# Kernel tuning notes

Hardware: AMD Instinct MI355X
Metric: run time of the kernel (lower is better)

Reference implementation:

```python
import jax, jax.numpy as jnp
import numpy as np

N = 40000      # num nodes (num_a + num_b)
DA = 128       # emb_size_a
DB = 128       # emb_size_b
E = 640000     # edges per sign (avg degree 16)
K = 3          # spectral_transform_layer
JA, JB = 1.0, 1.0  # Jacobi_paper (a, b)
EPS = 1e-5     # BatchNorm1d eps


def spmm(index, value, n, x):
    # torch_sparse.spmm: out[row] += value * x[col]
    row, col = index[0], index[1]
    return jax.ops.segment_sum(x[col] * value[:, None], row, num_segments=n)


def jacobi_last(x0, idx, val, k, a, b):
    # Jacobi polynomial basis recurrence; returns xs[k-1]
    n = x0.shape[0]
    xs = [x0]
    if k >= 2:
        x1 = ((a - b) / 2) * x0 + ((a + b + 2) / 2) * spmm(idx, val, n, x0)
        xs.append(x1)
    for L in range(2, k):
        c1 = (2 * L + a + b - 1) * (2 * L + a + b) / (2 * L) / (L + a + b)
        c2 = (2 * L + a + b - 1) * (a * a - b * b) / (2 * L) / (L + a + b) / (2 * L + a + b - 2)
        c3 = (L + a) * (L + b) * (2 * L + a + b) / L / (L + a + b) / (2 * L + a + b - 2)
        xn = c1 * spmm(idx, val, n, xs[-1]) + c2 * xs[-1] - c3 * xs[-2]
        xs.append(xn)
    return xs[-1]


def batchnorm(x, g, beta):
    # training-mode BatchNorm1d: batch stats, biased variance
    mu = jnp.mean(x, axis=0)
    var = jnp.var(x, axis=0)
    return g * (x - mu) * jax.lax.rsqrt(var + EPS) + beta


def prelu(x, w):
    return jnp.where(x >= 0, x, w * x)


def setup_inputs() -> dict:
    key = jax.random.key(0)
    ks = jax.random.split(key, 10)
    s = 1.0 / np.sqrt(DA)
    return {
        "x": jax.random.normal(ks[0], (N, DA), dtype=jnp.float32),
        "pos_index": jax.random.randint(ks[1], (2, E), 0, N, dtype=jnp.int64 if jax.config.jax_enable_x64 else jnp.int32),
        "pos_weight": jax.random.uniform(ks[2], (E,), dtype=jnp.float32),
        "neg_index": jax.random.randint(ks[3], (2, E), 0, N, dtype=jnp.int64 if jax.config.jax_enable_x64 else jnp.int32),
        "neg_weight": jax.random.uniform(ks[4], (E,), dtype=jnp.float32),
        "W_org": jax.random.uniform(ks[5], (DA, DB), jnp.float32, -s, s),
        "W_pos": jax.random.uniform(ks[6], (DA, DB), jnp.float32, -s, s),
        "W_neg": jax.random.uniform(ks[7], (DA, DB), jnp.float32, -s, s),
        "g_org": jnp.ones((DB,), jnp.float32), "b_org": jnp.zeros((DB,), jnp.float32),
        "g_pos": jnp.ones((DB,), jnp.float32), "b_pos": jnp.zeros((DB,), jnp.float32),
        "g_neg": jnp.ones((DB,), jnp.float32), "b_neg": jnp.zeros((DB,), jnp.float32),
        "prelu_w": jnp.full((1,), 0.25, jnp.float32),
        "W_mlp": jax.random.uniform(ks[8], (3 * DB, DB), jnp.float32, -1.0 / np.sqrt(3 * DB), 1.0 / np.sqrt(3 * DB)),
    }


def reference(x, pos_index, pos_weight, neg_index, neg_weight,
              W_org, W_pos, W_neg, g_org, b_org, g_pos, b_pos, g_neg, b_neg,
              prelu_w, W_mlp):
    x_org = x @ W_org                      # [N, DB]
    x_pos = x @ W_pos
    x_neg = x @ W_neg
    # dropout p=0 -> identity
    x_pos = jacobi_last(x_pos, pos_index, pos_weight, K, JA, JB)
    x_neg = jacobi_last(x_neg, neg_index, neg_weight, K, JA, JB)
    x_org = batchnorm(x_org, g_org, b_org)  # alpha3 = 1
    x_pos = batchnorm(x_pos, g_pos, b_pos)
    x_neg = batchnorm(x_neg, g_neg, b_neg)
    x_org = prelu(x_org, prelu_w)
    x_pos = prelu(x_pos, prelu_w)
    x_neg = prelu(x_neg, prelu_w)
    embs = jnp.concatenate([x_org, x_pos, x_neg], axis=1) @ W_mlp  # [N, DB]
    norm = jnp.maximum(jnp.linalg.norm(embs, axis=1, keepdims=True), 1e-12)
    return embs / norm
```

## Files before the change

### kernel.cpp

```cpp
#include <hip/hip_runtime.h>

#define NNODES 40000
#define NEDGE  640000
#define NBUCK  625
#define ECAP   1408
#define QSZ16  1280000
#define QSZU   640000
#define PCHUNK 4096
#define PBLKS  313

typedef __attribute__((ext_vector_type(8))) short bfrag;
typedef __attribute__((ext_vector_type(4))) float facc;

union bfu { bfrag v; uint u[4]; };

__device__ inline ushort f2bf(float f) {
    uint u = __float_as_uint(f);
    return (ushort)((u + 0x7FFFu + ((u >> 16) & 1u)) >> 16);
}
__device__ inline float bf2f(ushort h) {
    return __uint_as_float(((uint)h) << 16);
}
__device__ inline float blo(uint u) { return __uint_as_float(u << 16); }
__device__ inline float bhi(uint u) { return __uint_as_float(u & 0xFFFF0000u); }


__global__ __launch_bounds__(256) void partition_k(const int* __restrict__ pos_idx,
                                                   const float* __restrict__ pos_w,
                                                   const int* __restrict__ neg_idx,
                                                   const float* __restrict__ neg_w,
                                                   int* __restrict__ ecnt,
                                                   int2* __restrict__ edges) {
    __shared__ int lhist[2 * NBUCK];
    __shared__ int lbase[2 * NBUCK];
    __shared__ ushort rows_s[PCHUNK];
    long g0 = (long)blockIdx.x * PCHUNK;
    for (int i = threadIdx.x; i < 2 * NBUCK; i += 256) lhist[i] = 0;
    __syncthreads();
#pragma unroll
    for (int i = 0; i < 16; ++i) {
        long g = g0 + i * 256 + threadIdx.x;
        if (g < 2 * NEDGE) {
            int sign = g >= NEDGE;
            int e = (int)(g - (long)sign * NEDGE);
            int row = sign ? neg_idx[e] : pos_idx[e];
            rows_s[i * 256 + threadIdx.x] = (ushort)row;
            atomicAdd(&lhist[sign * NBUCK + (row >> 6)], 1);
        }
    }
    __syncthreads();
    for (int b = threadIdx.x; b < 2 * NBUCK; b += 256) {
        int c = lhist[b];
        lbase[b] = c ? atomicAdd(&ecnt[b], c) : 0;
        lhist[b] = 0;
    }
    __syncthreads();
#pragma unroll
    for (int i = 0; i < 16; ++i) {
        long g = g0 + i * 256 + threadIdx.x;
        if (g < 2 * NEDGE) {
            int sign = g >= NEDGE;
            int e = (int)(g - (long)sign * NEDGE);
            int row = rows_s[i * 256 + threadIdx.x];
            int col = sign ? neg_idx[NEDGE + e] : pos_idx[NEDGE + e];
            float wv = sign ? neg_w[e] : pos_w[e];
            int b = sign * NBUCK + (row >> 6);
            int off = lbase[b] + atomicAdd(&lhist[b], 1);
            if (off < ECAP)
                edges[(long)b * ECAP + off] =
                    make_int2((int)((uint)col | ((uint)(row & 63) << 16)), __float_as_int(wv));
        }
    }
}


__global__ __launch_bounds__(256) void bucket_csr_k(const int* __restrict__ ecnt,
                                                    const int2* __restrict__ edges,
                                                    uint* __restrict__ ecomp,
                                                    int2* __restrict__ rp2) {
    __shared__ int2 stage[ECAP];
    __shared__ int hist[64];
    __shared__ int base_[64];
    int b = blockIdx.x;
    int tid = threadIdx.x;
    int cnt = ecnt[b]; if (cnt > ECAP) cnt = ECAP;
    if (tid < 64) hist[tid] = 0;
    __syncthreads();
    long e0 = (long)b * ECAP;
    for (int i = tid; i < cnt; i += 256) {
        int2 e = edges[e0 + i];
        stage[i] = e;
        atomicAdd(&hist[((uint)e.x >> 16) & 63u], 1);
    }
    __syncthreads();
    if (tid < 64) {
        int v = hist[tid];
        int s = v;
#pragma unroll
        for (int off = 1; off < 64; off <<= 1) {
            int t = __shfl_up(s, off);
            if ((tid & 63) >= off) s += t;
        }
        int excl = s - v;
        base_[tid] = excl;
        int sign = b >= NBUCK;
        int r = (b - sign * NBUCK) * 64 + tid;
        rp2[sign * NNODES + r] = make_int2((int)(e0 + excl), (int)(e0 + excl + v));
        hist[tid] = 0;
    }
    __syncthreads();
    for (int i = tid; i < cnt; i += 256) {
        int2 e = stage[i];
        int rl = ((uint)e.x >> 16) & 63u;
        int pos = base_[rl] + atomicAdd(&hist[rl], 1);
        ecomp[e0 + pos] = ((uint)e.x & 0xFFFFu) |
                          ((uint)f2bf(__int_as_float(e.y)) << 16);
    }
}


__global__ __launch_bounds__(256) void pack_all_k(const float* __restrict__ Wo,
                                                  const float* __restrict__ Wp,
                                                  const float* __restrict__ Wn,
                                                  const float* __restrict__ Wm,
                                                  ushort* __restrict__ out) {
    int idx = blockIdx.x * 256 + threadIdx.x;
    const float* W;
    ushort* dst;
    int local;
    if (idx < 49152) {
        int m = idx >> 14;
        local = idx & 16383;
        W = (m == 0) ? Wo : (m == 1) ? Wp : Wn;
        dst = out + m * 16384;
    } else {
        local = idx - 49152;
        W = Wm;
        dst = out + 49152;
    }
    int j = local & 7, l = (local >> 3) & 63, t = (local >> 9) & 7, ks = local >> 12;
    int k = ks * 32 + (l >> 4) * 8 + j;
    int c = (l & 15) + 16 * t;
    dst[local] = f2bf(W[k * 128 + c]);
}


__global__ __launch_bounds__(256) void mfma_gemm3_k(const float* __restrict__ x,
                                                    const ushort* __restrict__ B0,
                                                    const ushort* __restrict__ B1,
                                                    const ushort* __restrict__ B2,
                                                    ushort* __restrict__ O0,
                                                    ushort* __restrict__ O1,
                                                    ushort* __restrict__ O2,
                                                    float* __restrict__ sums,
                                                    float* __restrict__ sumsq) {
    __shared__ float cs[128], cq[128];
    int tid = threadIdx.x;
    int lane = tid & 63, wave = tid >> 6;
    if (tid < 128) { cs[tid] = 0.f; cq[tid] = 0.f; }
    __syncthreads();
    long rbase = (long)blockIdx.x * 64 + wave * 16;
    int r = lane & 15, kg = lane >> 4;
    const float* xr = x + (rbase + r) * 128 + kg * 8;
    bfrag a[4];
#pragma unroll
    for (int ks = 0; ks < 4; ++ks) {
        float4 lo = *(const float4*)(xr + ks * 32);
        float4 hi = *(const float4*)(xr + ks * 32 + 4);
        bfu t;
        t.u[0] = (uint)f2bf(lo.x) | ((uint)f2bf(lo.y) << 16);
        t.u[1] = (uint)f2bf(lo.z) | ((uint)f2bf(lo.w) << 16);
        t.u[2] = (uint)f2bf(hi.x) | ((uint)f2bf(hi.y) << 16);
        t.u[3] = (uint)f2bf(hi.z) | ((uint)f2bf(hi.w) << 16);
        a[ks] = t.v;
    }
    const ushort* Bs[3] = {B0, B1, B2};
    ushort* Os[3] = {O0, O1, O2};
    long orow = rbase + kg * 4;
#pragma unroll
    for (int m = 0; m < 3; ++m) {
        const bfrag* Bq = (const bfrag*)Bs[m] + lane;
        facc acc[8];
#pragma unroll
        for (int t = 0; t < 8; ++t) acc[t] = (facc){0.f, 0.f, 0.f, 0.f};
#pragma unroll
        for (int ks = 0; ks < 4; ++ks)
#pragma unroll
            for (int t = 0; t < 8; ++t)
                acc[t] = __builtin_amdgcn_mfma_f32_16x16x32_bf16(a[ks], Bq[(ks * 8 + t) * 64], acc[t], 0, 0, 0);
        ushort* O = Os[m];
#pragma unroll
        for (int t = 0; t < 8; ++t) {
            float s_ = 0.f, q_ = 0.f;
            long qb = (long)(t >> 1) * QSZ16 + (t & 1) * 16 + r;
#pragma unroll
            for (int j = 0; j < 4; ++j) {
                ushort bv = f2bf(acc[t][j]);
                O[qb + (orow + j) * 32] = bv;
                if (m == 0) {
                    float fv = bf2f(bv);
                    s_ += fv;
                    q_ = fmaf(fv, fv, q_);
                }
            }
            if (m == 0) {
                atomicAdd(&cs[16 * t + r], s_);
                atomicAdd(&cq[16 * t + r], q_);
            }
        }
    }
    __syncthreads();
    if (tid < 128) {
        atomicAdd(&sums[tid], cs[tid]);
        atomicAdd(&sumsq[tid], cq[tid]);
    }
}


template<int PHASE>
__global__ __launch_bounds__(256) void spmmg_k(const int2* __restrict__ rp2,
                                               const uint* __restrict__ ec,
                                               const uint* __restrict__ p_in,
                                               const uint* __restrict__ n_in,
                                               const uint* __restrict__ p_prev,
                                               const uint* __restrict__ n_prev,
                                               uint* __restrict__ p_out,
                                               uint* __restrict__ n_out) {
    int grp = blockIdx.x & 7;
    int rg  = blockIdx.x >> 3;
    int sign = grp >> 2, q = grp & 3;
    int tid = threadIdx.x;
    int w = tid >> 6, lane = tid & 63;
    int u = lane & 7;
    int rl = lane >> 3;
    const uint2* in  = (const uint2*)((sign ? n_in : p_in) + q * QSZU);
    uint2* out = (uint2*)((sign ? n_out : p_out) + q * QSZU);
    int r = rg * 32 + w * 8 + rl;
    int2 se = rp2[sign * NNODES + r];
    float ax = 0.f, ay = 0.f, az = 0.f, aw = 0.f;
    float bx = 0.f, by = 0.f, bz = 0.f, bw = 0.f;
    int e = se.x, e1 = se.y;
    for (; e + 2 <= e1; e += 2) {
        uint ea = ec[e], eb = ec[e + 1];
        uint2 ga = in[(ea & 0xFFFFu) * 8 + u];
        uint2 gb = in[(eb & 0xFFFFu) * 8 + u];
        float wa = bhi(ea), wb = bhi(eb);
        ax = fmaf(wa, blo(ga.x), ax); ay = fmaf(wa, bhi(ga.x), ay);
        az = fmaf(wa, blo(ga.y), az); aw = fmaf(wa, bhi(ga.y), aw);
        bx = fmaf(wb, blo(gb.x), bx); by = fmaf(wb, bhi(gb.x), by);
        bz = fmaf(wb, blo(gb.y), bz); bw = fmaf(wb, bhi(gb.y), bw);
    }
    if (e < e1) {
        uint ea = ec[e];
        uint2 ga = in[(ea & 0xFFFFu) * 8 + u];
        float wa = bhi(ea);
        ax = fmaf(wa, blo(ga.x), ax); ay = fmaf(wa, bhi(ga.x), ay);
        az = fmaf(wa, blo(ga.y), az); aw = fmaf(wa, bhi(ga.y), aw);
    }
    ax += bx; ay += by; az += bz; aw += bw;
    uint2 res;
    if (PHASE == 1) {
        res.x = (uint)f2bf(2.f * ax) | ((uint)f2bf(2.f * ay) << 16);
        res.y = (uint)f2bf(2.f * az) | ((uint)f2bf(2.f * aw) << 16);
    } else {
        const uint2* prev = (const uint2*)((sign ? n_prev : p_prev) + q * QSZU);
        uint2 pu = prev[r * 8 + u];
        float rx = fmaf(1.875f, ax, -1.6875f * blo(pu.x));
        float ry = fmaf(1.875f, ay, -1.6875f * bhi(pu.x));
        float rz = fmaf(1.875f, az, -1.6875f * blo(pu.y));
        float rw = fmaf(1.875f, aw, -1.6875f * bhi(pu.y));
        res.x = (uint)f2bf(rx) | ((uint)f2bf(ry) << 16);
        res.y = (uint)f2bf(rz) | ((uint)f2bf(rw) << 16);
    }
    out[r * 8 + u] = res;
}


__global__ __launch_bounds__(256) void stats2_k(const ushort* __restrict__ pos,
                                                const ushort* __restrict__ neg,
                                                float* __restrict__ sums,
                                                float* __restrict__ sumsq) {
    int b = blockIdx.x;
    int sign = b >= 313;
    int blk = b - sign * 313;
    const ushort* buf = sign ? neg : pos;
    int c = threadIdx.x & 127, half = threadIdx.x >> 7;
    int qq = c >> 5, cc = c & 31;
    const ushort* base = buf + (long)qq * QSZ16 + cc;
    int r0 = blk * 128;
    int rend = r0 + 128; if (rend > NNODES) rend = NNODES;
    float s = 0.f, s2 = 0.f;
    for (int r = r0 + half; r < rend; r += 2) {
        float v = bf2f(base[r * 32]);
        s += v;
        s2 = fmaf(v, v, s2);
    }
    __shared__ float sh[256], sh2[256];
    sh[threadIdx.x] = s; sh2[threadIdx.x] = s2;
    __syncthreads();
    if (threadIdx.x < 128) {
        int sb = 128 + sign * 128;
        atomicAdd(&sums[sb + c],  sh[c]  + sh[c + 128]);
        atomicAdd(&sumsq[sb + c], sh2[c] + sh2[c + 128]);
    }
}

__global__ void bnfin_k(const float* __restrict__ sum, const float* __restrict__ sumsq,
                        const float* __restrict__ g0, const float* __restrict__ be0,
                        const float* __restrict__ g1, const float* __restrict__ be1,
                        const float* __restrict__ g2, const float* __restrict__ be2,
                        float* __restrict__ bn) {
    int i = threadIdx.x;
    if (i >= 384) return;
    int s = i >> 7, c = i & 127;
    float mean = sum[i] * (1.f / NNODES);
    float var  = sumsq[i] * (1.f / NNODES) - mean * mean;
    const float* g = (s == 0) ? g0 : (s == 1) ? g1 : g2;
    const float* b = (s == 0) ? be0 : (s == 1) ? be1 : be2;
    float sc = g[c] * rsqrtf(var + 1e-5f);
    bn[s * 256 + c]       = sc;
    bn[s * 256 + 128 + c] = b[c] - mean * sc;
}


__global__ __launch_bounds__(256) void mfma_gemm_mlp_k(const ushort* __restrict__ org,
                                                       const ushort* __restrict__ pos,
                                                       const ushort* __restrict__ neg,
                                                       const float* __restrict__ bn,
                                                       const float* __restrict__ prelu_w,
                                                       const ushort* __restrict__ Bp,
                                                       float* __restrict__ Out) {
    int lane = threadIdx.x & 63, wave = threadIdx.x >> 6;
    long rbase = (long)blockIdx.x * 64 + wave * 16;
    int r = lane & 15, kg = lane >> 4;
    float pw = prelu_w[0];
    facc acc[8];
#pragma unroll
    for (int t = 0; t < 8; ++t) acc[t] = (facc){0.f, 0.f, 0.f, 0.f};
    const bfrag* Bq = (const bfrag*)Bp + lane;
#pragma unroll
    for (int ks = 0; ks < 12; ++ks) {
        int c = ks * 32 + kg * 8;
        int s = c >> 7;
        int off = c & 127;
        const ushort* src = (s == 0) ? org : (s == 1) ? pos : neg;
        const uint* srcu = (const uint*)src;
        uint4 u = *(const uint4*)(srcu + (long)(off >> 5) * QSZU + (rbase + r) * 16 + ((off & 31) >> 1));
        float4 sc_lo = *(const float4*)(bn + s * 256 + off);
        float4 sc_hi = *(const float4*)(bn + s * 256 + off + 4);
        float4 sh_lo = *(const float4*)(bn + s * 256 + 128 + off);
        float4 sh_hi = *(const float4*)(bn + s * 256 + 128 + off + 4);
        uint uu[4] = {u.x, u.y, u.z, u.w};
        float scv[8] = {sc_lo.x, sc_lo.y, sc_lo.z, sc_lo.w, sc_hi.x, sc_hi.y, sc_hi.z, sc_hi.w};
        float shv[8] = {sh_lo.x, sh_lo.y, sh_lo.z, sh_lo.w, sh_hi.x, sh_hi.y, sh_hi.z, sh_hi.w};
        bfu av;
#pragma unroll
        for (int k = 0; k < 4; ++k) {
            float vx = __uint_as_float(uu[k] << 16);
            float vy = __uint_as_float(uu[k] & 0xFFFF0000u);
            float ox = fmaf(vx, scv[2 * k],     shv[2 * k]);     ox = (ox >= 0.f) ? ox : pw * ox;
            float oy = fmaf(vy, scv[2 * k + 1], shv[2 * k + 1]); oy = (oy >= 0.f) ? oy : pw * oy;
            av.u[k] = (uint)f2bf(ox) | ((uint)f2bf(oy) << 16);
        }
#pragma unroll
        for (int t = 0; t < 8; ++t)
            acc[t] = __builtin_amdgcn_mfma_f32_16x16x32_bf16(av.v, Bq[(ks * 8 + t) * 64], acc[t], 0, 0, 0);
    }
    long orow = rbase + kg * 4;
#pragma unroll
    for (int j = 0; j < 4; ++j) {
        float ss = 0.f;
#pragma unroll
        for (int t = 0; t < 8; ++t) ss = fmaf(acc[t][j], acc[t][j], ss);
        ss += __shfl_xor(ss, 1);
        ss += __shfl_xor(ss, 2);
        ss += __shfl_xor(ss, 4);
        ss += __shfl_xor(ss, 8);
        float inv = 1.f / fmaxf(sqrtf(ss), 1e-12f);
#pragma unroll
        for (int t = 0; t < 8; ++t)
            Out[(orow + j) * 128 + 16 * t + r] = acc[t][j] * inv;
    }
}


extern "C" void kernel_launch(void* const* d_in, const int* in_sizes, int n_in,
                              void* d_out, int out_size, void* d_ws, size_t ws_size,
                              hipStream_t stream) {
    const float* x       = (const float*)d_in[0];
    const int*   pos_idx = (const int*)d_in[1];
    const float* pos_w   = (const float*)d_in[2];
    const int*   neg_idx = (const int*)d_in[3];
    const float* neg_w   = (const float*)d_in[4];
    const float* W_org   = (const float*)d_in[5];
    const float* W_pos   = (const float*)d_in[6];
    const float* W_neg   = (const float*)d_in[7];
    const float* g_org   = (const float*)d_in[8];
    const float* b_org   = (const float*)d_in[9];
    const float* g_pos   = (const float*)d_in[10];
    const float* b_pos   = (const float*)d_in[11];
    const float* g_neg   = (const float*)d_in[12];
    const float* b_neg   = (const float*)d_in[13];
    const float* prelu_w = (const float*)d_in[14];
    const float* W_mlp   = (const float*)d_in[15];
    float* out = (float*)d_out;

    char* ws = (char*)d_ws;
    const size_t FB = (size_t)NNODES * 128 * 2;
    ushort* org0b = (ushort*)(ws);
    ushort* p0b   = (ushort*)(ws + FB);
    ushort* n0b   = (ushort*)(ws + 2 * FB);
    int2* edges   = (int2*)(ws + 3 * FB);
    uint* ecomp   = (uint*)(ws + 3 * FB + 14080000);
    char* small   = ws + 3 * FB + 14080000 + 7040000;
    int* ecnt     = (int*)small;
    float* sums   = (float*)(small + 5120);
    float* sumsq  = (float*)(small + 5120 + 1536);
    float* bn     = (float*)(small + 8192);
    int2* rp2     = (int2*)(small + 8192 + 3072);
    ushort* Wb    = (ushort*)(small + 8192 + 3072 + 640000);
    uint* t1_pos  = (uint*)d_out;
    uint* t1_neg  = (uint*)d_out + 4 * QSZU;

    hipMemsetAsync(small, 0, 8192, stream);

    partition_k<<<PBLKS, 256, 0, stream>>>(pos_idx, pos_w, neg_idx, neg_w, ecnt, edges);
    bucket_csr_k<<<2 * NBUCK, 256, 0, stream>>>(ecnt, edges, ecomp, rp2);
    pack_all_k<<<384, 256, 0, stream>>>(W_org, W_pos, W_neg, W_mlp, Wb);

    mfma_gemm3_k<<<625, 256, 0, stream>>>(x, Wb, Wb + 16384, Wb + 32768,
                                          org0b, p0b, n0b, sums, sumsq);

    spmmg_k<1><<<10000, 256, 0, stream>>>(rp2, ecomp,
        (const uint*)p0b, (const uint*)n0b, nullptr, nullptr, t1_pos, t1_neg);
    spmmg_k<2><<<10000, 256, 0, stream>>>(rp2, ecomp,
        t1_pos, t1_neg, (const uint*)p0b, (const uint*)n0b, (uint*)p0b, (uint*)n0b);

    stats2_k<<<626, 256, 0, stream>>>(p0b, n0b, sums, sumsq);
    bnfin_k<<<1, 384, 0, stream>>>(sums, sumsq, g_org, b_org, g_pos, b_pos, g_neg, b_neg, bn);
    mfma_gemm_mlp_k<<<625, 256, 0, stream>>>(org0b, p0b, n0b, bn, prelu_w, Wb + 49152, out);

    (void)in_sizes; (void)n_in; (void)out_size; (void)ws_size;
}
```

Before: 223.9 us.

## Fuse weight packing, BN statistics and BN finalize into neighboring kernels; unroll SpMM by 4

Merges the weight-packing kernel into the edge partition kernel as extra blocks. BatchNorm sum and sum-of-squares are now accumulated in the epilogue of the second SpMM pass through shared-memory atomics, and the finalize step is recomputed per block inside the MLP GEMM. The SpMM edge loop is also unrolled to four independent gathers with separate accumulators. Together these remove three launches and one full re-read of the propagated features, at the cost of shared atomic contention, redundant per-block BN finalization, and higher register pressure.

```diff
diff --git a/kernel.cpp b/kernel.cpp
--- a/kernel.cpp
+++ b/kernel.cpp
@@ -25,15 +25,41 @@
 __device__ inline float bhi(uint u) { return __uint_as_float(u & 0xFFFF0000u); }
 
 
-__global__ __launch_bounds__(256) void partition_k(const int* __restrict__ pos_idx,
-                                                   const float* __restrict__ pos_w,
-                                                   const int* __restrict__ neg_idx,
-                                                   const float* __restrict__ neg_w,
-                                                   int* __restrict__ ecnt,
-                                                   int2* __restrict__ edges) {
+__global__ __launch_bounds__(256) void prep_k(const int* __restrict__ pos_idx,
+                                              const float* __restrict__ pos_w,
+                                              const int* __restrict__ neg_idx,
+                                              const float* __restrict__ neg_w,
+                                              int* __restrict__ ecnt,
+                                              int2* __restrict__ edges,
+                                              const float* __restrict__ Wo,
+                                              const float* __restrict__ Wp,
+                                              const float* __restrict__ Wn,
+                                              const float* __restrict__ Wm,
+                                              ushort* __restrict__ wout) {
     __shared__ int lhist[2 * NBUCK];
     __shared__ int lbase[2 * NBUCK];
     __shared__ ushort rows_s[PCHUNK];
+    if (blockIdx.x >= PBLKS) {
+        int idx = (blockIdx.x - PBLKS) * 256 + threadIdx.x;
+        const float* W;
+        ushort* dst;
+        int local;
+        if (idx < 49152) {
+            int m = idx >> 14;
+            local = idx & 16383;
+            W = (m == 0) ? Wo : (m == 1) ? Wp : Wn;
+            dst = wout + m * 16384;
+        } else {
+            local = idx - 49152;
+            W = Wm;
+            dst = wout + 49152;
+        }
+        int j = local & 7, l = (local >> 3) & 63, t = (local >> 9) & 7, ks = local >> 12;
+        int k = ks * 32 + (l >> 4) * 8 + j;
+        int c = (l & 15) + 16 * t;
+        dst[local] = f2bf(W[k * 128 + c]);
+        return;
+    }
     long g0 = (long)blockIdx.x * PCHUNK;
     for (int i = threadIdx.x; i < 2 * NBUCK; i += 256) lhist[i] = 0;
     __syncthreads();
@@ -119,32 +145,6 @@
 }
 
 
-__global__ __launch_bounds__(256) void pack_all_k(const float* __restrict__ Wo,
-                                                  const float* __restrict__ Wp,
-                                                  const float* __restrict__ Wn,
-                                                  const float* __restrict__ Wm,
-                                                  ushort* __restrict__ out) {
-    int idx = blockIdx.x * 256 + threadIdx.x;
-    const float* W;
-    ushort* dst;
-    int local;
-    if (idx < 49152) {
-        int m = idx >> 14;
-        local = idx & 16383;
-        W = (m == 0) ? Wo : (m == 1) ? Wp : Wn;
-        dst = out + m * 16384;
-    } else {
-        local = idx - 49152;
-        W = Wm;
-        dst = out + 49152;
-    }
-    int j = local & 7, l = (local >> 3) & 63, t = (local >> 9) & 7, ks = local >> 12;
-    int k = ks * 32 + (l >> 4) * 8 + j;
-    int c = (l & 15) + 16 * t;
-    dst[local] = f2bf(W[k * 128 + c]);
-}
-
-
 __global__ __launch_bounds__(256) void mfma_gemm3_k(const float* __restrict__ x,
                                                     const ushort* __restrict__ B0,
                                                     const ushort* __restrict__ B1,
@@ -225,7 +225,10 @@
                                                const uint* __restrict__ p_prev,
                                                const uint* __restrict__ n_prev,
                                                uint* __restrict__ p_out,
-                                               uint* __restrict__ n_out) {
+                                               uint* __restrict__ n_out,
+                                               float* __restrict__ sums,
+                                               float* __restrict__ sumsq) {
+    __shared__ float lsum[32], lsq[32];
     int grp = blockIdx.x & 7;
     int rg  = blockIdx.x >> 3;
     int sign = grp >> 2, q = grp & 3;
@@ -233,14 +236,33 @@
     int w = tid >> 6, lane = tid & 63;
     int u = lane & 7;
     int rl = lane >> 3;
+    if (PHASE == 2 && tid < 32) { lsum[tid] = 0.f; lsq[tid] = 0.f; }
     const uint2* in  = (const uint2*)((sign ? n_in : p_in) + q * QSZU);
     uint2* out = (uint2*)((sign ? n_out : p_out) + q * QSZU);
     int r = rg * 32 + w * 8 + rl;
     int2 se = rp2[sign * NNODES + r];
     float ax = 0.f, ay = 0.f, az = 0.f, aw = 0.f;
     float bx = 0.f, by = 0.f, bz = 0.f, bw = 0.f;
+    float cx = 0.f, cy = 0.f, cz = 0.f, cw = 0.f;
+    float dx = 0.f, dy = 0.f, dz = 0.f, dw = 0.f;
     int e = se.x, e1 = se.y;
-    for (; e + 2 <= e1; e += 2) {
+    for (; e + 4 <= e1; e += 4) {
+        uint ea = ec[e], eb = ec[e + 1], ecc = ec[e + 2], edd = ec[e + 3];
+        uint2 ga = in[(ea  & 0xFFFFu) * 8 + u];
+        uint2 gb = in[(eb  & 0xFFFFu) * 8 + u];
+        uint2 gc = in[(ecc & 0xFFFFu) * 8 + u];
+        uint2 gd = in[(edd & 0xFFFFu) * 8 + u];
+        float wa = bhi(ea), wb = bhi(eb), wc = bhi(ecc), wd = bhi(edd);
+        ax = fmaf(wa, blo(ga.x), ax); ay = fmaf(wa, bhi(ga.x), ay);
+        az = fmaf(wa, blo(ga.y), az); aw = fmaf(wa, bhi(ga.y), aw);
+        bx = fmaf(wb, blo(gb.x), bx); by = fmaf(wb, bhi(gb.x), by);
+        bz = fmaf(wb, blo(gb.y), bz); bw = fmaf(wb, bhi(gb.y), bw);
+        cx = fmaf(wc, blo(gc.x), cx); cy = fmaf(wc, bhi(gc.x), cy);
+        cz = fmaf(wc, blo(gc.y), cz); cw = fmaf(wc, bhi(gc.y), cw);
+        dx = fmaf(wd, blo(gd.x), dx); dy = fmaf(wd, bhi(gd.x), dy);
+        dz = fmaf(wd, blo(gd.y), dz); dw = fmaf(wd, bhi(gd.y), dw);
+    }
+    if (e + 2 <= e1) {
         uint ea = ec[e], eb = ec[e + 1];
         uint2 ga = in[(ea & 0xFFFFu) * 8 + u];
         uint2 gb = in[(eb & 0xFFFFu) * 8 + u];
@@ -249,6 +271,7 @@
         az = fmaf(wa, blo(ga.y), az); aw = fmaf(wa, bhi(ga.y), aw);
         bx = fmaf(wb, blo(gb.x), bx); by = fmaf(wb, bhi(gb.x), by);
         bz = fmaf(wb, blo(gb.y), bz); bw = fmaf(wb, bhi(gb.y), bw);
+        e += 2;
     }
     if (e < e1) {
         uint ea = ec[e];
@@ -257,11 +280,13 @@
         ax = fmaf(wa, blo(ga.x), ax); ay = fmaf(wa, bhi(ga.x), ay);
         az = fmaf(wa, blo(ga.y), az); aw = fmaf(wa, bhi(ga.y), aw);
     }
-    ax += bx; ay += by; az += bz; aw += bw;
+    ax += bx + cx + dx; ay += by + cy + dy;
+    az += bz + cz + dz; aw += bw + cw + dw;
     uint2 res;
     if (PHASE == 1) {
         res.x = (uint)f2bf(2.f * ax) | ((uint)f2bf(2.f * ay) << 16);
         res.y = (uint)f2bf(2.f * az) | ((uint)f2bf(2.f * aw) << 16);
+        out[r * 8 + u] = res;
     } else {
         const uint2* prev = (const uint2*)((sign ? n_prev : p_prev) + q * QSZU);
         uint2 pu = prev[r * 8 + u];
@@ -271,66 +296,52 @@
         float rw = fmaf(1.875f, aw, -1.6875f * bhi(pu.y));
         res.x = (uint)f2bf(rx) | ((uint)f2bf(ry) << 16);
         res.y = (uint)f2bf(rz) | ((uint)f2bf(rw) << 16);
-    }
-    out[r * 8 + u] = res;
-}
-
-
-__global__ __launch_bounds__(256) void stats2_k(const ushort* __restrict__ pos,
-                                                const ushort* __restrict__ neg,
-                                                float* __restrict__ sums,
-                                                float* __restrict__ sumsq) {
-    int b = blockIdx.x;
-    int sign = b >= 313;
-    int blk = b - sign * 313;
-    const ushort* buf = sign ? neg : pos;
-    int c = threadIdx.x & 127, half = threadIdx.x >> 7;
-    int qq = c >> 5, cc = c & 31;
-    const ushort* base = buf + (long)qq * QSZ16 + cc;
-    int r0 = blk * 128;
-    int rend = r0 + 128; if (rend > NNODES) rend = NNODES;
-    float s = 0.f, s2 = 0.f;
-    for (int r = r0 + half; r < rend; r += 2) {
-        float v = bf2f(base[r * 32]);
-        s += v;
-        s2 = fmaf(v, v, s2);
-    }
-    __shared__ float sh[256], sh2[256];
-    sh[threadIdx.x] = s; sh2[threadIdx.x] = s2;
-    __syncthreads();
-    if (threadIdx.x < 128) {
-        int sb = 128 + sign * 128;
-        atomicAdd(&sums[sb + c],  sh[c]  + sh[c + 128]);
-        atomicAdd(&sumsq[sb + c], sh2[c] + sh2[c + 128]);
-    }
-}
-
-__global__ void bnfin_k(const float* __restrict__ sum, const float* __restrict__ sumsq,
-                        const float* __restrict__ g0, const float* __restrict__ be0,
-                        const float* __restrict__ g1, const float* __restrict__ be1,
-                        const float* __restrict__ g2, const float* __restrict__ be2,
-                        float* __restrict__ bn) {
-    int i = threadIdx.x;
-    if (i >= 384) return;
-    int s = i >> 7, c = i & 127;
-    float mean = sum[i] * (1.f / NNODES);
-    float var  = sumsq[i] * (1.f / NNODES) - mean * mean;
-    const float* g = (s == 0) ? g0 : (s == 1) ? g1 : g2;
-    const float* b = (s == 0) ? be0 : (s == 1) ? be1 : be2;
-    float sc = g[c] * rsqrtf(var + 1e-5f);
-    bn[s * 256 + c]       = sc;
-    bn[s * 256 + 128 + c] = b[c] - mean * sc;
+        out[r * 8 + u] = res;
+        float fx = blo(res.x), fy = bhi(res.x);
+        float fz = blo(res.y), fw = bhi(res.y);
+        __syncthreads();
+        atomicAdd(&lsum[4 * u + 0], fx); atomicAdd(&lsq[4 * u + 0], fx * fx);
+        atomicAdd(&lsum[4 * u + 1], fy); atomicAdd(&lsq[4 * u + 1], fy * fy);
+        atomicAdd(&lsum[4 * u + 2], fz); atomicAdd(&lsq[4 * u + 2], fz * fz);
+        atomicAdd(&lsum[4 * u + 3], fw); atomicAdd(&lsq[4 * u + 3], fw * fw);
+        __syncthreads();
+        if (tid < 32) {
+            int gch = 128 + sign * 128 + q * 32 + tid;
+            atomicAdd(&sums[gch],  lsum[tid]);
+            atomicAdd(&sumsq[gch], lsq[tid]);
+        }
+    }
 }
 
 
 __global__ __launch_bounds__(256) void mfma_gemm_mlp_k(const ushort* __restrict__ org,
                                                        const ushort* __restrict__ pos,
                                                        const ushort* __restrict__ neg,
-                                                       const float* __restrict__ bn,
+                                                       const float* __restrict__ sums,
+                                                       const float* __restrict__ sumsq,
+                                                       const float* __restrict__ g0,
+                                                       const float* __restrict__ be0,
+                                                       const float* __restrict__ g1,
+                                                       const float* __restrict__ be1,
+                                                       const float* __restrict__ g2,
+                                                       const float* __restrict__ be2,
                                                        const float* __restrict__ prelu_w,
                                                        const ushort* __restrict__ Bp,
                                                        float* __restrict__ Out) {
-    int lane = threadIdx.x & 63, wave = threadIdx.x >> 6;
+    __shared__ __align__(16) float bnl[768];
+    int tid = threadIdx.x;
+    for (int i = tid; i < 384; i += 256) {
+        int s = i >> 7, c = i & 127;
+        float mean = sums[i] * (1.f / NNODES);
+        float var  = sumsq[i] * (1.f / NNODES) - mean * mean;
+        const float* g = (s == 0) ? g0 : (s == 1) ? g1 : g2;
+        const float* b = (s == 0) ? be0 : (s == 1) ? be1 : be2;
+        float sc = g[c] * rsqrtf(var + 1e-5f);
+        bnl[s * 256 + c]       = sc;
+        bnl[s * 256 + 128 + c] = b[c] - mean * sc;
+    }
+    __syncthreads();
+    int lane = tid & 63, wave = tid >> 6;
     long rbase = (long)blockIdx.x * 64 + wave * 16;
     int r = lane & 15, kg = lane >> 4;
     float pw = prelu_w[0];
@@ -346,10 +357,10 @@
         const ushort* src = (s == 0) ? org : (s == 1) ? pos : neg;
         const uint* srcu = (const uint*)src;
         uint4 u = *(const uint4*)(srcu + (long)(off >> 5) * QSZU + (rbase + r) * 16 + ((off & 31) >> 1));
-        float4 sc_lo = *(const float4*)(bn + s * 256 + off);
-        float4 sc_hi = *(const float4*)(bn + s * 256 + off + 4);
-        float4 sh_lo = *(const float4*)(bn + s * 256 + 128 + off);
-        float4 sh_hi = *(const float4*)(bn + s * 256 + 128 + off + 4);
+        float4 sc_lo = *(const float4*)(bnl + s * 256 + off);
+        float4 sc_hi = *(const float4*)(bnl + s * 256 + off + 4);
+        float4 sh_lo = *(const float4*)(bnl + s * 256 + 128 + off);
+        float4 sh_hi = *(const float4*)(bnl + s * 256 + 128 + off + 4);
         uint uu[4] = {u.x, u.y, u.z, u.w};
         float scv[8] = {sc_lo.x, sc_lo.y, sc_lo.z, sc_lo.w, sc_hi.x, sc_hi.y, sc_hi.z, sc_hi.w};
         float shv[8] = {sh_lo.x, sh_lo.y, sh_lo.z, sh_lo.w, sh_hi.x, sh_hi.y, sh_hi.z, sh_hi.w};
@@ -416,29 +427,30 @@
     int* ecnt     = (int*)small;
     float* sums   = (float*)(small + 5120);
     float* sumsq  = (float*)(small + 5120 + 1536);
-    float* bn     = (float*)(small + 8192);
-    int2* rp2     = (int2*)(small + 8192 + 3072);
-    ushort* Wb    = (ushort*)(small + 8192 + 3072 + 640000);
+    int2* rp2     = (int2*)(small + 8192);
+    ushort* Wb    = (ushort*)(small + 8192 + 640000);
     uint* t1_pos  = (uint*)d_out;
     uint* t1_neg  = (uint*)d_out + 4 * QSZU;
 
     hipMemsetAsync(small, 0, 8192, stream);
 
-    partition_k<<<PBLKS, 256, 0, stream>>>(pos_idx, pos_w, neg_idx, neg_w, ecnt, edges);
+    prep_k<<<PBLKS + 384, 256, 0, stream>>>(pos_idx, pos_w, neg_idx, neg_w, ecnt, edges,
+                                            W_org, W_pos, W_neg, W_mlp, Wb);
     bucket_csr_k<<<2 * NBUCK, 256, 0, stream>>>(ecnt, edges, ecomp, rp2);
-    pack_all_k<<<384, 256, 0, stream>>>(W_org, W_pos, W_neg, W_mlp, Wb);
 
     mfma_gemm3_k<<<625, 256, 0, stream>>>(x, Wb, Wb + 16384, Wb + 32768,
                                           org0b, p0b, n0b, sums, sumsq);
 
     spmmg_k<1><<<10000, 256, 0, stream>>>(rp2, ecomp,
-        (const uint*)p0b, (const uint*)n0b, nullptr, nullptr, t1_pos, t1_neg);
+        (const uint*)p0b, (const uint*)n0b, nullptr, nullptr, t1_pos, t1_neg,
+        sums, sumsq);
     spmmg_k<2><<<10000, 256, 0, stream>>>(rp2, ecomp,
-        t1_pos, t1_neg, (const uint*)p0b, (const uint*)n0b, (uint*)p0b, (uint*)n0b);
-
-    stats2_k<<<626, 256, 0, stream>>>(p0b, n0b, sums, sumsq);
-    bnfin_k<<<1, 384, 0, stream>>>(sums, sumsq, g_org, b_org, g_pos, b_pos, g_neg, b_neg, bn);
-    mfma_gemm_mlp_k<<<625, 256, 0, stream>>>(org0b, p0b, n0b, bn, prelu_w, Wb + 49152, out);
+        t1_pos, t1_neg, (const uint*)p0b, (const uint*)n0b, (uint*)p0b, (uint*)n0b,
+        sums, sumsq);
+
+    mfma_gemm_mlp_k<<<625, 256, 0, stream>>>(org0b, p0b, n0b, sums, sumsq,
+                                             g_org, b_org, g_pos, b_pos, g_neg, b_neg,
+                                             prelu_w, Wb + 49152, out);
 
     (void)in_sizes; (void)n_in; (void)out_size; (void)ws_size;
 }
```

Result: slower. 277.8 us (+24.0%).
